# Optimization experiments

Measured on AMD Instinct MI355X. Metric: run time of the kernel, lower is better.

## Reference

```python
import jax, jax.numpy as jnp
from jax import lax
import numpy as np

B, L = 8192, 16384
DILATIONS = (1, 4, 8, 32, 128)
ALPHA = 0.3  # Keras LeakyReLU default


def _conv_same(x, w, b, d):
    # x: [B, steps, C_in], w: [k, C_in, C_out], SAME padding with rhs dilation d
    y = lax.conv_general_dilated(
        x, w, window_strides=(1,), padding='SAME', rhs_dilation=(d,),
        dimension_numbers=('NWC', 'WIO', 'NWC'))
    return y + b


def _leaky(x):
    return jnp.where(x >= 0, x, ALPHA * x)


def setup_inputs() -> dict:
    key = jax.random.key(0)
    ks = jax.random.split(key, 8)
    x = jax.random.normal(ks[0], (B, L), dtype=jnp.float32)
    # c1: kernel_size=2, in_channels=L, filters=1
    w1 = jax.random.normal(ks[1], (2, L, 1), dtype=jnp.float32) * 0.02
    b1 = jnp.zeros((1,), dtype=jnp.float32)
    # c2..c5: in_channels=1, filters=1
    w2 = jax.random.normal(ks[2], (2, 1, 1), dtype=jnp.float32) * 0.5
    b2 = jnp.zeros((1,), dtype=jnp.float32)
    w3 = jax.random.normal(ks[3], (2, 1, 1), dtype=jnp.float32) * 0.5
    b3 = jnp.zeros((1,), dtype=jnp.float32)
    w4 = jax.random.normal(ks[4], (2, 1, 1), dtype=jnp.float32) * 0.5
    b4 = jnp.zeros((1,), dtype=jnp.float32)
    w5 = jax.random.normal(ks[5], (2, 1, 1), dtype=jnp.float32) * 0.5
    b5 = jnp.zeros((1,), dtype=jnp.float32)
    # Dense(128) applied to last dim (size 1)
    wd = jax.random.normal(ks[6], (1, 128), dtype=jnp.float32) * 0.5
    bd = jnp.zeros((128,), dtype=jnp.float32)
    return {"x": x, "w1": w1, "b1": b1, "w2": w2, "b2": b2, "w3": w3,
            "b3": b3, "w4": w4, "b4": b4, "w5": w5, "b5": b5,
            "wd": wd, "bd": bd}


def reference(x, w1, b1, w2, b2, w3, b3, w4, b4, w5, b5, wd, bd):
    xe = x[:, None, :]                       # [B, 1, L] (steps=1, channels=L)
    c1 = _conv_same(xe, w1, b1, DILATIONS[0])  # [B, 1, 1]
    c2 = _conv_same(_leaky(c1), w2, b2, DILATIONS[1])
    c3 = _conv_same(_leaky(c2), w3, b3, DILATIONS[2])
    c4 = _conv_same(_leaky(c3), w4, b4, DILATIONS[3])
    c5 = _conv_same(_leaky(c4), w5, b5, DILATIONS[4])
    s = c1 + c2 + c3 + c4 + c5               # [B, 1, 1]
    out = jnp.einsum('bsc,cd->bsd', s, wd) + bd  # [B, 1, 128]
    return jnp.squeeze(out)                  # [B, 128]
```

## Files before the change

kernel.cpp:

```cpp
#include <hip/hip_runtime.h>


constexpr int L    = 16384;
constexpr int OUTD = 128;
constexpr int ROWS_PER_BLOCK = 4;

typedef float fx4 __attribute__((ext_vector_type(4)));

__global__ __launch_bounds__(256)
void audio_collapse_kernel(const float* __restrict__ x,
                           const float* __restrict__ w1,
                           const float* __restrict__ b1,
                           const float* __restrict__ b2,
                           const float* __restrict__ b3,
                           const float* __restrict__ b4,
                           const float* __restrict__ b5,
                           const float* __restrict__ wd,
                           const float* __restrict__ bd,
                           float* __restrict__ out,
                           int B)
{
    const int wave = threadIdx.x >> 6;
    const int lane = threadIdx.x & 63;
    const int row  = blockIdx.x * ROWS_PER_BLOCK + wave;
    if (row >= B) return;

    const fx4* __restrict__ xr = (const fx4*)(x + (size_t)row * L);
    const fx4* __restrict__ wr = (const fx4*)(w1);

    float acc0 = 0.f, acc1 = 0.f, acc2 = 0.f, acc3 = 0.f;
    #pragma unroll
    for (int k = 0; k < L / 4 / 256; ++k) {
        const int base = k * 256 + lane;
        fx4 xv0 = __builtin_nontemporal_load(&xr[base]);
        fx4 xv1 = __builtin_nontemporal_load(&xr[base +  64]);
        fx4 xv2 = __builtin_nontemporal_load(&xr[base + 128]);
        fx4 xv3 = __builtin_nontemporal_load(&xr[base + 192]);
        fx4 wv0 = wr[base];
        fx4 wv1 = wr[base +  64];
        fx4 wv2 = wr[base + 128];
        fx4 wv3 = wr[base + 192];
        acc0 += xv0.x * wv0.x + xv0.y * wv0.y + xv0.z * wv0.z + xv0.w * wv0.w;
        acc1 += xv1.x * wv1.x + xv1.y * wv1.y + xv1.z * wv1.z + xv1.w * wv1.w;
        acc2 += xv2.x * wv2.x + xv2.y * wv2.y + xv2.z * wv2.z + xv2.w * wv2.w;
        acc3 += xv3.x * wv3.x + xv3.y * wv3.y + xv3.z * wv3.z + xv3.w * wv3.w;
    }
    float acc = (acc0 + acc1) + (acc2 + acc3);

    #pragma unroll
    for (int off = 32; off > 0; off >>= 1)
        acc += __shfl_xor(acc, off, 64);

    const float y = acc + b1[0] + b2[0] + b3[0] + b4[0] + b5[0];

    float* __restrict__ orow = out + (size_t)row * OUTD;
    #pragma unroll
    for (int j = lane; j < OUTD; j += 64)
        __builtin_nontemporal_store(fmaf(y, wd[j], bd[j]), &orow[j]);
}

extern "C" void kernel_launch(void* const* d_in, const int* in_sizes, int n_in,
                              void* d_out, int out_size, void* d_ws, size_t ws_size,
                              hipStream_t stream) {
    const float* x  = (const float*)d_in[0];
    const float* w1 = (const float*)d_in[1];
    const float* b1 = (const float*)d_in[2];
    const float* b2 = (const float*)d_in[4];
    const float* b3 = (const float*)d_in[6];
    const float* b4 = (const float*)d_in[8];
    const float* b5 = (const float*)d_in[10];
    const float* wd = (const float*)d_in[11];
    const float* bd = (const float*)d_in[12];
    float* out = (float*)d_out;

    const int B = in_sizes[0] / L;
    const int grid = (B + ROWS_PER_BLOCK - 1) / ROWS_PER_BLOCK;

    audio_collapse_kernel<<<grid, 256, 0, stream>>>(
        x, w1, b1, b2, b3, b4, b5, wd, bd, out, B);
}
```

Measured before the change: 674.1 us.

## Assign one row per 256-thread block with all loads issued up front

Each row is now reduced by a whole 256-thread block instead of a single wavefront. Every thread loads all 16 x and weight vectors into registers before any arithmetic, which raises memory-level parallelism. The four wave partial sums are combined through shared memory and a block barrier. This adds register pressure (launch_bounds with min 2 blocks) and a sync per row, but shortens per-row latency and spreads the 512MB stream across more concurrent requests.

```diff
diff --git a/kernel.cpp b/kernel.cpp
--- a/kernel.cpp
+++ b/kernel.cpp
@@ -3,11 +3,11 @@
 
 constexpr int L    = 16384;
 constexpr int OUTD = 128;
-constexpr int ROWS_PER_BLOCK = 4;
+constexpr int VPT  = 16;
 
 typedef float fx4 __attribute__((ext_vector_type(4)));
 
-__global__ __launch_bounds__(256)
+__global__ __launch_bounds__(256, 2)
 void audio_collapse_kernel(const float* __restrict__ x,
                            const float* __restrict__ w1,
                            const float* __restrict__ b1,
@@ -20,43 +20,46 @@
                            float* __restrict__ out,
                            int B)
 {
-    const int wave = threadIdx.x >> 6;
-    const int lane = threadIdx.x & 63;
-    const int row  = blockIdx.x * ROWS_PER_BLOCK + wave;
+    const int tid = threadIdx.x;
+    const int row = blockIdx.x;
     if (row >= B) return;
 
     const fx4* __restrict__ xr = (const fx4*)(x + (size_t)row * L);
     const fx4* __restrict__ wr = (const fx4*)(w1);
 
-    float acc0 = 0.f, acc1 = 0.f, acc2 = 0.f, acc3 = 0.f;
+    fx4 wv[VPT];
     #pragma unroll
-    for (int k = 0; k < L / 4 / 256; ++k) {
-        const int base = k * 256 + lane;
-        fx4 xv0 = __builtin_nontemporal_load(&xr[base]);
-        fx4 xv1 = __builtin_nontemporal_load(&xr[base +  64]);
-        fx4 xv2 = __builtin_nontemporal_load(&xr[base + 128]);
-        fx4 xv3 = __builtin_nontemporal_load(&xr[base + 192]);
-        fx4 wv0 = wr[base];
-        fx4 wv1 = wr[base +  64];
-        fx4 wv2 = wr[base + 128];
-        fx4 wv3 = wr[base + 192];
-        acc0 += xv0.x * wv0.x + xv0.y * wv0.y + xv0.z * wv0.z + xv0.w * wv0.w;
-        acc1 += xv1.x * wv1.x + xv1.y * wv1.y + xv1.z * wv1.z + xv1.w * wv1.w;
-        acc2 += xv2.x * wv2.x + xv2.y * wv2.y + xv2.z * wv2.z + xv2.w * wv2.w;
-        acc3 += xv3.x * wv3.x + xv3.y * wv3.y + xv3.z * wv3.z + xv3.w * wv3.w;
-    }
-    float acc = (acc0 + acc1) + (acc2 + acc3);
+    for (int k = 0; k < VPT; ++k)
+        wv[k] = wr[k * 256 + tid];
+
+    fx4 xv[VPT];
+    #pragma unroll
+    for (int k = 0; k < VPT; ++k)
+        xv[k] = __builtin_nontemporal_load(&xr[k * 256 + tid]);
+
+    float acc = 0.f;
+    #pragma unroll
+    for (int k = 0; k < VPT; ++k)
+        acc += xv[k].x * wv[k].x + xv[k].y * wv[k].y
+             + xv[k].z * wv[k].z + xv[k].w * wv[k].w;
 
     #pragma unroll
     for (int off = 32; off > 0; off >>= 1)
         acc += __shfl_xor(acc, off, 64);
 
-    const float y = acc + b1[0] + b2[0] + b3[0] + b4[0] + b5[0];
+    __shared__ float wsum[4];
+    const int wave = tid >> 6;
+    const int lane = tid & 63;
+    if (lane == 0) wsum[wave] = acc;
+    __syncthreads();
 
-    float* __restrict__ orow = out + (size_t)row * OUTD;
-    #pragma unroll
-    for (int j = lane; j < OUTD; j += 64)
-        __builtin_nontemporal_store(fmaf(y, wd[j], bd[j]), &orow[j]);
+    const float y = (wsum[0] + wsum[1]) + (wsum[2] + wsum[3])
+                  + b1[0] + b2[0] + b3[0] + b4[0] + b5[0];
+
+    if (tid < OUTD) {
+        float* __restrict__ orow = out + (size_t)row * OUTD;
+        __builtin_nontemporal_store(fmaf(y, wd[tid], bd[tid]), &orow[tid]);
+    }
 }
 
 extern "C" void kernel_launch(void* const* d_in, const int* in_sizes, int n_in,
@@ -74,8 +77,7 @@
     float* out = (float*)d_out;
 
     const int B = in_sizes[0] / L;
-    const int grid = (B + ROWS_PER_BLOCK - 1) / ROWS_PER_BLOCK;
 
-    audio_collapse_kernel<<<grid, 256, 0, stream>>>(
+    audio_collapse_kernel<<<B, 256, 0, stream>>>(
         x, w1, b1, b2, b3, b4, b5, wd, bd, out, B);
 }
```

After: 667.8 us. No clear change (-0.9%).
